# Optimization experiments

Measured on AMD Instinct MI355X. Metric: run time of the kernel, lower is better.

## Reference

```python
import jax, jax.numpy as jnp
import numpy as np

MAX_DISP = 40  # search range -> D = 2*MAX_DISP+1 = 81 cost channels
STRIDE = 1


def setup_inputs() -> dict:
    key = jax.random.key(0)
    k1, k2 = jax.random.split(key)
    B, C, H, W = 4, 256, 128, 416
    left = jax.random.normal(k1, (B, C, H, W), dtype=jnp.float32)
    right = jax.random.normal(k2, (B, C, H, W), dtype=jnp.float32)
    return {"left": left, "right": right}


def reference(left, right):
    # mode='time', reduction='mean': per horizontal shift i, cost = mean_C(left * shift(right, i))
    B, C, H, W = left.shape
    rp = jnp.pad(right, ((0, 0), (0, 0), (0, 0), (MAX_DISP, MAX_DISP)))  # [B,C,H,W+2M]
    costs = []
    for i in range(-MAX_DISP, MAX_DISP + 1, STRIDE):  # fixed small unrolled loop over 81 shifts
        sl = jax.lax.dynamic_slice_in_dim(rp, i + MAX_DISP, W, axis=3)  # [B,C,H,W]
        costs.append(jnp.mean(left * sl, axis=1, keepdims=True))        # [B,1,H,W]
    return jnp.concatenate(costs, axis=1)  # [B, 81, H, W]
```

## Files before the change

### kernel.cpp

```cpp
#include <hip/hip_runtime.h>
#include <hip/hip_bf16.h>
#include <stdint.h>

typedef __bf16 bf16x8 __attribute__((ext_vector_type(8)));
typedef float f32x4 __attribute__((ext_vector_type(4)));

#define MAXD 40
#define ND   81
#define CSZ  256
#define HSZ  128
#define WSZ  416
#define HW   (HSZ * WSZ)
#define NCHUNK 8

#define LSTR 448
#define RSTR 544
#define ROFF 14336
#define ESTR 420

static __device__ __forceinline__ void lds_barrier() {
    asm volatile("s_waitcnt lgkmcnt(0)" ::: "memory");
    __builtin_amdgcn_s_barrier();
    __builtin_amdgcn_sched_barrier(0);
}

__global__ __launch_bounds__(512, 2)
void corr_mfma_kernel(const float* __restrict__ left,
                      const float* __restrict__ right,
                      float* __restrict__ out) {
    __shared__ float Sh[31744];

    const int t   = threadIdx.x;
    const int wv  = t >> 6;
    const int l   = t & 63;
    const int l15 = l & 15;
    const int l4  = l >> 4;
    const int b   = blockIdx.x >> 7;
    const int h   = blockIdx.x & 127;

    int gq[7], lwL[7], lwR[7];
    #pragma unroll
    for (int i = 0; i < 7; ++i) {
        const int qi = i * 512 + t;
        const int c  = qi / 104;
        const int q  = qi - 104 * c;
        const int sh = 8 * ((c >> 3) & 3);
        gq[i]  = c * HW + 4 * q;
        lwL[i] = c * LSTR + sh + 4 * q;
        lwR[i] = ROFF + c * RSTR + sh + 40 + 4 * q;
    }

    #pragma unroll
    for (int i = 0; i < 5; ++i) {
        const int idx = i * 512 + t;
        const int c   = idx / 80;
        const int k   = idx - 80 * c;
        const int col = (k < 40) ? k : (k + 416);
        Sh[ROFF + c * RSTR + 8 * ((c >> 3) & 3) + col] = 0.0f;
    }

    f32x4 acc[4][6];
    #pragma unroll
    for (int pi = 0; pi < 4; ++pi)
        #pragma unroll
        for (int a = 0; a < 6; ++a)
            acc[pi][a] = (f32x4)0.0f;

    const size_t slab = ((size_t)b * CSZ) * HW + (size_t)h * WSZ;
    const float* Lp = left  + slab;
    const float* Rp = right + slab;

    const int LA = 3592 * l4 + l15;
    const int LB = ROFF + 4360 * l4 + l15;

    f32x4 vL[7], vR[7];

    #pragma unroll
    for (int i = 0; i < 7; ++i) {
        const int qi = i * 512 + t;
        if (qi < 3328) {
            vL[i] = *(const f32x4*)(Lp + gq[i]);
            vR[i] = *(const f32x4*)(Rp + gq[i]);
        }
    }
    #pragma unroll
    for (int i = 0; i < 7; ++i) {
        const int qi = i * 512 + t;
        if (qi < 3328) {
            *(f32x4*)&Sh[lwL[i]] = vL[i];
            *(f32x4*)&Sh[lwR[i]] = vR[i];
        }
    }
    lds_barrier();

    for (int ck = 0; ck < NCHUNK; ++ck) {
        const bool more = (ck + 1 < NCHUNK);

        if (more) {
            const float* Lc = Lp + (size_t)(ck + 1) * 32 * HW;
            const float* Rc = Rp + (size_t)(ck + 1) * 32 * HW;
            #pragma unroll
            for (int i = 0; i < 7; ++i) {
                const int qi = i * 512 + t;
                if (qi < 3328) {
                    vL[i] = *(const f32x4*)(Lc + gq[i]);
                    vR[i] = *(const f32x4*)(Rc + gq[i]);
                }
            }
        }

        bf16x8 bf[4];
        #pragma unroll
        for (int pi = 0; pi < 4; ++pi) {
            const int p = 4 * wv + pi;
            if (p <= 30) {
                #pragma unroll
                for (int kk = 0; kk < 8; ++kk)
                    bf[pi][kk] = (__bf16)Sh[LB + kk * RSTR + 16 * p];
            } else {
                #pragma unroll
                for (int kk = 0; kk < 8; ++kk) bf[pi][kk] = (__bf16)0.0f;
            }
        }
        #pragma unroll
        for (int s = 0; s < 9; ++s) {
            const int r = 4 * wv - 5 + s;
            if (r >= 0 && r <= 25) {
                bf16x8 af;
                #pragma unroll
                for (int kk = 0; kk < 8; ++kk)
                    af[kk] = (__bf16)Sh[LA + kk * LSTR + 16 * r];
                #pragma unroll
                for (int pi = 0; pi < 4; ++pi) {
                    const int a = s - pi;
                    if (a >= 0 && a <= 5)
                        acc[pi][a] = __builtin_amdgcn_mfma_f32_16x16x32_bf16(af, bf[pi], acc[pi][a], 0, 0, 0);
                }
            }
        }

        if (more) {
            lds_barrier();

            #pragma unroll
            for (int i = 0; i < 7; ++i) {
                const int qi = i * 512 + t;
                if (qi < 3328) {
                    *(f32x4*)&Sh[lwL[i]] = vL[i];
                    *(f32x4*)&Sh[lwR[i]] = vR[i];
                }
            }

            lds_barrier();
        }
    }

    lds_barrier();

    const float scale = 1.0f / 256.0f;
    float* outp = out + ((size_t)b * ND) * HW + (size_t)h * WSZ;

    #pragma unroll
    for (int half = 0; half < 2; ++half) {
        const int d0 = half * 41;
        const int dN = half ? 40 : 41;

        #pragma unroll
        for (int pi = 0; pi < 4; ++pi) {
            #pragma unroll
            for (int a = 0; a < 6; ++a) {
                const int r = 4 * wv + pi - 5 + a;
                if (r >= 0 && r <= 25) {
                    const int j = 5 - a;
                    #pragma unroll
                    for (int rr = 0; rr < 4; ++rr) {
                        const int m = 4 * l4 + rr;
                        const int d = 16 * j + l15 - m;
                        if (d >= d0 && d < d0 + dN)
                            Sh[(d - d0) * ESTR + 16 * r + m] = acc[pi][a][rr] * scale;
                    }
                }
            }
        }
        lds_barrier();

        #pragma unroll
        for (int i = 0; i < 9; ++i) {
            const int idx = i * 512 + t;
            if (idx < dN * 104) {
                const int d = idx / 104;
                const int q = idx - 104 * d;
                const f32x4 v = *(const f32x4*)&Sh[d * ESTR + 4 * q];
                *(f32x4*)(outp + (size_t)(d0 + d) * HW + 4 * q) = v;
            }
        }
        lds_barrier();
    }
}

extern "C" void kernel_launch(void* const* d_in, const int* in_sizes, int n_in,
                              void* d_out, int out_size, void* d_ws, size_t ws_size,
                              hipStream_t stream) {
    const float* left  = (const float*)d_in[0];
    const float* right = (const float*)d_in[1];
    float* out = (float*)d_out;
    (void)in_sizes; (void)n_in; (void)out_size; (void)d_ws; (void)ws_size;
    corr_mfma_kernel<<<dim3(4 * 128), dim3(512), 0, stream>>>(left, right, out);
}
```

Before: 109.4 us.

## Store bf16-packed channel pairs in LDS to shrink footprint and raise occupancy

Inputs are now converted to bf16 and packed as channel pairs when staged into shared memory, so LDS holds half the bytes and the fragment loads become four 32-bit reads instead of eight scalar float reads with conversion. This cuts LDS use from about 124KB to about 59KB, allowing launch bounds of 4 blocks per CU, and the epilogue is split into three groups of 27 disparities to fit the smaller buffer. The register prefetch double-buffering of the next chunk is removed in favour of relying on the extra occupancy to hide global load latency. The risks are serialized load-then-compute within each block and more register pressure from the higher occupancy target.

```diff
diff --git a/kernel.cpp b/kernel.cpp
--- a/kernel.cpp
+++ b/kernel.cpp
@@ -13,10 +13,19 @@
 #define HW   (HSZ * WSZ)
 #define NCHUNK 8
 
-#define LSTR 448
-#define RSTR 544
-#define ROFF 14336
-#define ESTR 420
+#define STRL  420
+#define STRR  500
+#define RBASE 6720
+#define SHDW  14720
+#define ESTR  420
+
+union FragU { uint32_t u[4]; bf16x8 v; };
+
+static __device__ __forceinline__ uint32_t pk2(float a, float b) {
+    union { __bf16 h[2]; uint32_t u; } v;
+    v.h[0] = (__bf16)a; v.h[1] = (__bf16)b;
+    return v.u;
+}
 
 static __device__ __forceinline__ void lds_barrier() {
     asm volatile("s_waitcnt lgkmcnt(0)" ::: "memory");
@@ -24,11 +33,11 @@
     __builtin_amdgcn_sched_barrier(0);
 }
 
-__global__ __launch_bounds__(512, 2)
+__global__ __launch_bounds__(512, 4)
 void corr_mfma_kernel(const float* __restrict__ left,
                       const float* __restrict__ right,
                       float* __restrict__ out) {
-    __shared__ float Sh[31744];
+    __shared__ uint32_t Sh[SHDW];
 
     const int t   = threadIdx.x;
     const int wv  = t >> 6;
@@ -38,25 +47,19 @@
     const int b   = blockIdx.x >> 7;
     const int h   = blockIdx.x & 127;
 
-    int gq[7], lwL[7], lwR[7];
-    #pragma unroll
-    for (int i = 0; i < 7; ++i) {
-        const int qi = i * 512 + t;
-        const int c  = qi / 104;
-        const int q  = qi - 104 * c;
-        const int sh = 8 * ((c >> 3) & 3);
-        gq[i]  = c * HW + 4 * q;
-        lwL[i] = c * LSTR + sh + 4 * q;
-        lwR[i] = ROFF + c * RSTR + sh + 40 + 4 * q;
-    }
+    const size_t slab = ((size_t)b * CSZ) * HW + (size_t)h * WSZ;
+    const float* Lp = left  + slab;
+    const float* Rp = right + slab;
 
     #pragma unroll
-    for (int i = 0; i < 5; ++i) {
+    for (int i = 0; i < 3; ++i) {
         const int idx = i * 512 + t;
-        const int c   = idx / 80;
-        const int k   = idx - 80 * c;
-        const int col = (k < 40) ? k : (k + 416);
-        Sh[ROFF + c * RSTR + 8 * ((c >> 3) & 3) + col] = 0.0f;
+        if (idx < 1280) {
+            const int cp = idx / 80;
+            const int k  = idx - 80 * cp;
+            const int col = (k < 40) ? k : (k + 416);
+            Sh[RBASE + cp * STRR + col] = 0u;
+        }
     }
 
     f32x4 acc[4][6];
@@ -66,118 +69,86 @@
         for (int a = 0; a < 6; ++a)
             acc[pi][a] = (f32x4)0.0f;
 
-    const size_t slab = ((size_t)b * CSZ) * HW + (size_t)h * WSZ;
-    const float* Lp = left  + slab;
-    const float* Rp = right + slab;
-
-    const int LA = 3592 * l4 + l15;
-    const int LB = ROFF + 4360 * l4 + l15;
-
-    f32x4 vL[7], vR[7];
-
-    #pragma unroll
-    for (int i = 0; i < 7; ++i) {
-        const int qi = i * 512 + t;
-        if (qi < 3328) {
-            vL[i] = *(const f32x4*)(Lp + gq[i]);
-            vR[i] = *(const f32x4*)(Rp + gq[i]);
-        }
-    }
-    #pragma unroll
-    for (int i = 0; i < 7; ++i) {
-        const int qi = i * 512 + t;
-        if (qi < 3328) {
-            *(f32x4*)&Sh[lwL[i]] = vL[i];
-            *(f32x4*)&Sh[lwR[i]] = vR[i];
-        }
-    }
-    lds_barrier();
+    const int LA = (4 * l4) * STRL + l15;
+    const int LB = RBASE + (4 * l4) * STRR + l15;
 
     for (int ck = 0; ck < NCHUNK; ++ck) {
-        const bool more = (ck + 1 < NCHUNK);
+        const float* Lc = Lp + (size_t)(ck * 32) * HW;
+        const float* Rc = Rp + (size_t)(ck * 32) * HW;
 
-        if (more) {
-            const float* Lc = Lp + (size_t)(ck + 1) * 32 * HW;
-            const float* Rc = Rp + (size_t)(ck + 1) * 32 * HW;
-            #pragma unroll
-            for (int i = 0; i < 7; ++i) {
-                const int qi = i * 512 + t;
-                if (qi < 3328) {
-                    vL[i] = *(const f32x4*)(Lc + gq[i]);
-                    vR[i] = *(const f32x4*)(Rc + gq[i]);
-                }
+        #pragma unroll
+        for (int i = 0; i < 7; ++i) {
+            const int idx = i * 512 + t;
+            if (idx < 3328) {
+                const int cp = idx / 208;
+                const int wp = idx - 208 * cp;
+                const float2 a0 = *(const float2*)(Lc + (size_t)(2 * cp) * HW + 2 * wp);
+                const float2 a1 = *(const float2*)(Lc + (size_t)(2 * cp + 1) * HW + 2 * wp);
+                const float2 b0 = *(const float2*)(Rc + (size_t)(2 * cp) * HW + 2 * wp);
+                const float2 b1 = *(const float2*)(Rc + (size_t)(2 * cp + 1) * HW + 2 * wp);
+                uint2 lw, rw;
+                lw.x = pk2(a0.x, a1.x);  lw.y = pk2(a0.y, a1.y);
+                rw.x = pk2(b0.x, b1.x);  rw.y = pk2(b0.y, b1.y);
+                *(uint2*)&Sh[cp * STRL + 2 * wp]              = lw;
+                *(uint2*)&Sh[RBASE + cp * STRR + 40 + 2 * wp] = rw;
             }
         }
+
+        lds_barrier();
 
         bf16x8 bf[4];
         #pragma unroll
         for (int pi = 0; pi < 4; ++pi) {
-            const int p = 4 * wv + pi;
-            if (p <= 30) {
-                #pragma unroll
-                for (int kk = 0; kk < 8; ++kk)
-                    bf[pi][kk] = (__bf16)Sh[LB + kk * RSTR + 16 * p];
-            } else {
-                #pragma unroll
-                for (int kk = 0; kk < 8; ++kk) bf[pi][kk] = (__bf16)0.0f;
-            }
+            const int p  = 4 * wv + pi;
+            const int pc = (p > 30) ? 30 : p;
+            FragU u;
+            #pragma unroll
+            for (int i2 = 0; i2 < 4; ++i2)
+                u.u[i2] = Sh[LB + i2 * STRR + 16 * pc];
+            bf[pi] = u.v;
         }
         #pragma unroll
         for (int s = 0; s < 9; ++s) {
             const int r = 4 * wv - 5 + s;
             if (r >= 0 && r <= 25) {
-                bf16x8 af;
+                FragU u;
                 #pragma unroll
-                for (int kk = 0; kk < 8; ++kk)
-                    af[kk] = (__bf16)Sh[LA + kk * LSTR + 16 * r];
+                for (int i2 = 0; i2 < 4; ++i2)
+                    u.u[i2] = Sh[LA + i2 * STRL + 16 * r];
+                const bf16x8 af = u.v;
                 #pragma unroll
                 for (int pi = 0; pi < 4; ++pi) {
                     const int a = s - pi;
-                    if (a >= 0 && a <= 5)
+                    if (a >= 0 && a <= 5 && (4 * wv + pi) <= 30)
                         acc[pi][a] = __builtin_amdgcn_mfma_f32_16x16x32_bf16(af, bf[pi], acc[pi][a], 0, 0, 0);
                 }
             }
         }
 
-        if (more) {
-            lds_barrier();
-
-            #pragma unroll
-            for (int i = 0; i < 7; ++i) {
-                const int qi = i * 512 + t;
-                if (qi < 3328) {
-                    *(f32x4*)&Sh[lwL[i]] = vL[i];
-                    *(f32x4*)&Sh[lwR[i]] = vR[i];
-                }
-            }
-
-            lds_barrier();
-        }
+        lds_barrier();
     }
 
-    lds_barrier();
-
+    float* Shf = (float*)Sh;
     const float scale = 1.0f / 256.0f;
     float* outp = out + ((size_t)b * ND) * HW + (size_t)h * WSZ;
 
-    #pragma unroll
-    for (int half = 0; half < 2; ++half) {
-        const int d0 = half * 41;
-        const int dN = half ? 40 : 41;
+    for (int g = 0; g < 3; ++g) {
+        const int d0 = 27 * g;
 
         #pragma unroll
         for (int pi = 0; pi < 4; ++pi) {
+            const int p = 4 * wv + pi;
             #pragma unroll
             for (int a = 0; a < 6; ++a) {
-                const int r = 4 * wv + pi - 5 + a;
+                const int r = p - 5 + a;
                 if (r >= 0 && r <= 25) {
                     const int j = 5 - a;
                     #pragma unroll
                     for (int rr = 0; rr < 4; ++rr) {
                         const int m = 4 * l4 + rr;
                         const int d = 16 * j + l15 - m;
-                        if (d >= d0 && d < d0 + dN)
-                            Sh[(d - d0) * ESTR + 16 * r + m] = acc[pi][a][rr] * scale;
+                        if (d >= d0 && d < d0 + 27)
+                            Shf[(d - d0) * ESTR + 16 * r + m] = acc[pi][a][rr] * scale;
                     }
                 }
             }
@@ -185,16 +156,16 @@
         lds_barrier();
 
         #pragma unroll
-        for (int i = 0; i < 9; ++i) {
+        for (int i = 0; i < 6; ++i) {
             const int idx = i * 512 + t;
-            if (idx < dN * 104) {
+            if (idx < 27 * 104) {
                 const int d = idx / 104;
                 const int q = idx - 104 * d;
-                const f32x4 v = *(const f32x4*)&Sh[d * ESTR + 4 * q];
+                const f32x4 v = *(const f32x4*)&Shf[d * ESTR + 4 * q];
                 *(f32x4*)(outp + (size_t)(d0 + d) * HW + 4 * q) = v;
             }
         }
-        lds_barrier();
+        if (g < 2) lds_barrier();
     }
 }
 
```

Result: slower. 250.9 us (+129.4%).

## Double block size to 1024 threads with two column tiles per wave

Applied to the files above, without the earlier changes.

Raises the block from 512 to 1024 threads (16 waves), so each wave owns two right-image column tiles instead of four. Per-thread accumulators, prefetch registers and address arrays shrink, which is meant to lower register pressure and raise the number of waves available for latency hiding. The epilogue is re-split into three 27-disparity groups to fit the LDS staging buffer. The cost is that the left-tile A fragments are reloaded and converted across more waves, which adds LDS traffic, and the launch-bounds hint of 4 blocks per SM may be unattainable given the large shared-memory allocation.

```diff
diff --git a/kernel.cpp b/kernel.cpp
--- a/kernel.cpp
+++ b/kernel.cpp
@@ -24,7 +24,7 @@
     __builtin_amdgcn_sched_barrier(0);
 }
 
-__global__ __launch_bounds__(512, 2)
+__global__ __launch_bounds__(1024, 4)
 void corr_mfma_kernel(const float* __restrict__ left,
                       const float* __restrict__ right,
                       float* __restrict__ out) {
@@ -38,57 +38,55 @@
     const int b   = blockIdx.x >> 7;
     const int h   = blockIdx.x & 127;
 
-    int gq[7], lwL[7], lwR[7];
-    #pragma unroll
-    for (int i = 0; i < 7; ++i) {
-        const int qi = i * 512 + t;
-        const int c  = qi / 104;
-        const int q  = qi - 104 * c;
-        const int sh = 8 * ((c >> 3) & 3);
-        gq[i]  = c * HW + 4 * q;
-        lwL[i] = c * LSTR + sh + 4 * q;
-        lwR[i] = ROFF + c * RSTR + sh + 40 + 4 * q;
-    }
-
-    #pragma unroll
-    for (int i = 0; i < 5; ++i) {
-        const int idx = i * 512 + t;
-        const int c   = idx / 80;
-        const int k   = idx - 80 * c;
-        const int col = (k < 40) ? k : (k + 416);
-        Sh[ROFF + c * RSTR + 8 * ((c >> 3) & 3) + col] = 0.0f;
-    }
-
-    f32x4 acc[4][6];
-    #pragma unroll
-    for (int pi = 0; pi < 4; ++pi)
-        #pragma unroll
-        for (int a = 0; a < 6; ++a)
-            acc[pi][a] = (f32x4)0.0f;
-
     const size_t slab = ((size_t)b * CSZ) * HW + (size_t)h * WSZ;
     const float* Lp = left  + slab;
     const float* Rp = right + slab;
 
+    #pragma unroll
+    for (int i = 0; i < 3; ++i) {
+        const int idx = i * 1024 + t;
+        if (idx < 2560) {
+            const int c = idx / 80;
+            const int k = idx - 80 * c;
+            const int col = (k < 40) ? k : (k + 416);
+            Sh[ROFF + c * RSTR + 8 * ((c >> 3) & 3) + col] = 0.0f;
+        }
+    }
+
+    const int p0 = 2 * wv;
+    const bool hasP1 = (p0 + 1 <= 30);
+
+    f32x4 acc[2][6];
+    #pragma unroll
+    for (int pi = 0; pi < 2; ++pi)
+        #pragma unroll
+        for (int k = 0; k < 6; ++k)
+            acc[pi][k] = (f32x4)0.0f;
+
     const int LA = 3592 * l4 + l15;
     const int LB = ROFF + 4360 * l4 + l15;
 
-    f32x4 vL[7], vR[7];
-
-    #pragma unroll
-    for (int i = 0; i < 7; ++i) {
-        const int qi = i * 512 + t;
-        if (qi < 3328) {
-            vL[i] = *(const f32x4*)(Lp + gq[i]);
-            vR[i] = *(const f32x4*)(Rp + gq[i]);
-        }
-    }
-    #pragma unroll
-    for (int i = 0; i < 7; ++i) {
-        const int qi = i * 512 + t;
-        if (qi < 3328) {
-            *(f32x4*)&Sh[lwL[i]] = vL[i];
-            *(f32x4*)&Sh[lwR[i]] = vR[i];
+    f32x4 vL[4], vR[4];
+
+    #pragma unroll
+    for (int i = 0; i < 4; ++i) {
+        const int idx = i * 1024 + t;
+        if (idx < 3328) {
+            const int c = idx / 104;
+            const int q = idx - 104 * c;
+            vL[i] = *(const f32x4*)(Lp + (size_t)c * HW + 4 * q);
+            vR[i] = *(const f32x4*)(Rp + (size_t)c * HW + 4 * q);
+        }
+    }
+    #pragma unroll
+    for (int i = 0; i < 4; ++i) {
+        const int idx = i * 1024 + t;
+        if (idx < 3328) {
+            const int c  = idx / 104;
+            const int q  = idx - 104 * c;
+            const int sh = 8 * ((c >> 3) & 3);
+            *(f32x4*)&Sh[c * LSTR + sh + 4 * q]             = vL[i];
+            *(f32x4*)&Sh[ROFF + c * RSTR + sh + 40 + 4 * q] = vR[i];
         }
     }
     lds_barrier();
@@ -100,42 +98,38 @@
             const float* Lc = Lp + (size_t)(ck + 1) * 32 * HW;
             const float* Rc = Rp + (size_t)(ck + 1) * 32 * HW;
             #pragma unroll
-            for (int i = 0; i < 7; ++i) {
-                const int qi = i * 512 + t;
-                if (qi < 3328) {
-                    vL[i] = *(const f32x4*)(Lc + gq[i]);
-                    vR[i] = *(const f32x4*)(Rc + gq[i]);
+            for (int i = 0; i < 4; ++i) {
+                const int idx = i * 1024 + t;
+                if (idx < 3328) {
+                    const int c = idx / 104;
+                    const int q = idx - 104 * c;
+                    vL[i] = *(const f32x4*)(Lc + (size_t)c * HW + 4 * q);
+                    vR[i] = *(const f32x4*)(Rc + (size_t)c * HW + 4 * q);
                 }
             }
         }
 
-        bf16x8 bf[4];
-        #pragma unroll
-        for (int pi = 0; pi < 4; ++pi) {
-            const int p = 4 * wv + pi;
-            if (p <= 30) {
-                #pragma unroll
-                for (int kk = 0; kk < 8; ++kk)
-                    bf[pi][kk] = (__bf16)Sh[LB + kk * RSTR + 16 * p];
-            } else {
-                #pragma unroll
-                for (int kk = 0; kk < 8; ++kk) bf[pi][kk] = (__bf16)0.0f;
-            }
-        }
-        #pragma unroll
-        for (int s = 0; s < 9; ++s) {
-            const int r = 4 * wv - 5 + s;
+        bf16x8 bfr[2];
+        #pragma unroll
+        for (int pi = 0; pi < 2; ++pi) {
+            const int p  = p0 + pi;
+            const int pc = (p > 30) ? 30 : p;
+            #pragma unroll
+            for (int kk = 0; kk < 8; ++kk)
+                bfr[pi][kk] = (__bf16)Sh[LB + kk * RSTR + 16 * pc];
+        }
+        #pragma unroll
+        for (int a = 0; a < 7; ++a) {
+            const int r = p0 - 5 + a;
             if (r >= 0 && r <= 25) {
                 bf16x8 af;
                 #pragma unroll
                 for (int kk = 0; kk < 8; ++kk)
                     af[kk] = (__bf16)Sh[LA + kk * LSTR + 16 * r];
-                #pragma unroll
-                for (int pi = 0; pi < 4; ++pi) {
-                    const int a = s - pi;
-                    if (a >= 0 && a <= 5)
-                        acc[pi][a] = __builtin_amdgcn_mfma_f32_16x16x32_bf16(af, bf[pi], acc[pi][a], 0, 0, 0);
-                }
+                if (a < 6)
+                    acc[0][a] = __builtin_amdgcn_mfma_f32_16x16x32_bf16(af, bfr[0], acc[0][a], 0, 0, 0);
+                if (hasP1 && a >= 1)
+                    acc[1][a - 1] = __builtin_amdgcn_mfma_f32_16x16x32_bf16(af, bfr[1], acc[1][a - 1], 0, 0, 0);
             }
         }
 
@@ -143,11 +137,14 @@
             lds_barrier();
 
             #pragma unroll
-            for (int i = 0; i < 7; ++i) {
-                const int qi = i * 512 + t;
-                if (qi < 3328) {
-                    *(f32x4*)&Sh[lwL[i]] = vL[i];
-                    *(f32x4*)&Sh[lwR[i]] = vR[i];
+            for (int i = 0; i < 4; ++i) {
+                const int idx = i * 1024 + t;
+                if (idx < 3328) {
+                    const int c  = idx / 104;
+                    const int q  = idx - 104 * c;
+                    const int sh = 8 * ((c >> 3) & 3);
+                    *(f32x4*)&Sh[c * LSTR + sh + 4 * q]             = vL[i];
+                    *(f32x4*)&Sh[ROFF + c * RSTR + sh + 40 + 4 * q] = vR[i];
                 }
             }
 
@@ -160,24 +157,22 @@
     const float scale = 1.0f / 256.0f;
     float* outp = out + ((size_t)b * ND) * HW + (size_t)h * WSZ;
 
-    #pragma unroll
-    for (int half = 0; half < 2; ++half) {
-        const int d0 = half * 41;
-        const int dN = half ? 40 : 41;
-
-        #pragma unroll
-        for (int pi = 0; pi < 4; ++pi) {
-            #pragma unroll
-            for (int a = 0; a < 6; ++a) {
-                const int r = 4 * wv + pi - 5 + a;
+    for (int g = 0; g < 3; ++g) {
+        const int d0 = 27 * g;
+
+        #pragma unroll
+        for (int pi = 0; pi < 2; ++pi) {
+            #pragma unroll
+            for (int k = 0; k < 6; ++k) {
+                const int r = p0 - 5 + pi + k;
                 if (r >= 0 && r <= 25) {
-                    const int j = 5 - a;
+                    const int j = 5 - k;
                     #pragma unroll
                     for (int rr = 0; rr < 4; ++rr) {
                         const int m = 4 * l4 + rr;
                         const int d = 16 * j + l15 - m;
-                        if (d >= d0 && d < d0 + dN)
-                            Sh[(d - d0) * ESTR + 16 * r + m] = acc[pi][a][rr] * scale;
+                        if (d >= d0 && d < d0 + 27)
+                            Sh[(d - d0) * ESTR + 16 * r + m] = acc[pi][k][rr] * scale;
                     }
                 }
             }
@@ -185,16 +180,16 @@
         lds_barrier();
 
         #pragma unroll
-        for (int i = 0; i < 9; ++i) {
-            const int idx = i * 512 + t;
-            if (idx < dN * 104) {
+        for (int i = 0; i < 3; ++i) {
+            const int idx = i * 1024 + t;
+            if (idx < 2808) {
                 const int d = idx / 104;
                 const int q = idx - 104 * d;
                 const f32x4 v = *(const f32x4*)&Sh[d * ESTR + 4 * q];
                 *(f32x4*)(outp + (size_t)(d0 + d) * HW + 4 * q) = v;
             }
         }
-        lds_barrier();
+        if (g < 2) lds_barrier();
     }
 }
 
@@ -205,5 +200,5 @@
     const float* right = (const float*)d_in[1];
     float* out = (float*)d_out;
     (void)in_sizes; (void)n_in; (void)out_size; (void)d_ws; (void)ws_size;
-    corr_mfma_kernel<<<dim3(4 * 128), dim3(512), 0, stream>>>(left, right, out);
+    corr_mfma_kernel<<<dim3(4 * 128), dim3(1024), 0, stream>>>(left, right, out);
 }
```

Measured after the change: 170.5 us. +55.9%, slower.
